# Kernel tuning notes

Measured on AMD Instinct MI355X. Metric: run time of the kernel, lower is better.

## Reference

```python
import jax, jax.numpy as jnp
import numpy as np

N_LAYERS = 10


def _rel_graph_conv(x, src, dst, etype, W_rel, W_loop, b):
    # x: [N, h]; W_rel: [R, h, h] (per-relation weight), DGL low_mem style:
    # project all nodes by all relations, then gather per edge by (etype, src).
    xr = jnp.einsum('ni,rio->rno', x, W_rel)          # [R, N, h]
    m = xr[etype, src]                                 # [E, h] per-edge messages
    agg = jax.ops.segment_sum(m, dst, num_segments=x.shape[0])  # sum aggregation
    # DGL RelGraphConv defaults: self_loop=True, bias=True, no activation
    return agg + x @ W_loop + b


def setup_inputs() -> dict:
    key = jax.random.key(0)
    ks = jax.random.split(key, 12)
    N, E, F, H, R = 100000, 600000, 64, 128, 8
    inp = {
        'feats': jax.random.normal(ks[0], (N, F), dtype=jnp.float32),
        'src': jax.random.randint(ks[1], (E,), 0, N, dtype=jnp.int32),
        'dst': jax.random.randint(ks[2], (E,), 0, N, dtype=jnp.int32),
        'etype': jax.random.randint(ks[3], (E,), 0, R, dtype=jnp.int32),
    }
    s = 0.05
    inp['W_in'] = jax.random.normal(ks[4], (F, H), dtype=jnp.float32) * s
    inp['b_in'] = jnp.zeros((H,), dtype=jnp.float32)
    # stacked params for 10 layer-dependent GCNConv layers
    inp['W_rel'] = jax.random.normal(ks[5], (N_LAYERS, R, H, H), dtype=jnp.float32) * s
    inp['W_loop'] = jax.random.normal(ks[6], (N_LAYERS, H, H), dtype=jnp.float32) * s
    inp['b_rel'] = jnp.zeros((N_LAYERS, H), dtype=jnp.float32)
    inp['W_u1'] = jax.random.normal(ks[7], (N_LAYERS, 2 * H, 2 * H), dtype=jnp.float32) * s  # Linear(h+h, 2h)
    inp['b_u1'] = jnp.zeros((N_LAYERS, 2 * H), dtype=jnp.float32)
    inp['W_u2'] = jax.random.normal(ks[8], (N_LAYERS, 3 * H, H), dtype=jnp.float32) * s      # Linear(h+2h, h)
    inp['b_u2'] = jnp.zeros((N_LAYERS, H), dtype=jnp.float32)
    return inp


def reference(feats, src, dst, etype, W_in, b_in, W_rel, W_loop, b_rel, W_u1, b_u1, W_u2, b_u2):
    act = jnp.tanh  # activation_dict['tanh']
    x = act(feats @ W_in + b_in)  # conv_input
    for l in range(N_LAYERS):
        msg = _rel_graph_conv(x, src, dst, etype, W_rel[l], W_loop[l], b_rel[l])
        mid = act(jnp.concatenate([x, msg], axis=1) @ W_u1[l] + b_u1[l])
        out = jnp.concatenate([x, mid], axis=1) @ W_u2[l] + b_u2[l]
        x = act(out)
    return x
```

## Files before the change

### kernel.cpp

```cpp
#include <hip/hip_runtime.h>
#include <cstddef>


#define HID 128
#define NREL 8
#define NL 10

typedef __attribute__((ext_vector_type(8))) __bf16 bf16x8;
typedef __attribute__((ext_vector_type(4))) float f32x4;

__device__ __forceinline__ float fast_tanh(float x) {
  float cx = fminf(fmaxf(x, -10.f), 10.f);
  float z = exp2f(cx * 2.8853900817779268f);
  return (z - 1.f) * __builtin_amdgcn_rcpf(z + 1.f);
}

__global__ __launch_bounds__(256) void k_transpose(const float* __restrict__ W,
                                                   __bf16* __restrict__ Wt,
                                                   int K, int Nc,
                                                   int inDiv, int inScale, int inOff,
                                                   int outDiv, int outScale, int outOff) {
  __shared__ float t[32][33];
  int z = blockIdx.z;
  int zi = (z / inDiv) * inScale + (z % inDiv) + inOff;
  int zo = (z / outDiv) * outScale + (z % outDiv) + outOff;
  const float* Wz = W + (size_t)zi * K * Nc;
  __bf16* Wtz = Wt + (size_t)zo * K * Nc;
  int n0 = blockIdx.x * 32, k0 = blockIdx.y * 32;
#pragma unroll
  for (int i = 0; i < 4; i++) {
    int k = k0 + threadIdx.y + i * 8;
    int n = n0 + threadIdx.x;
    t[threadIdx.y + i * 8][threadIdx.x] = Wz[(size_t)k * Nc + n];
  }
  __syncthreads();
#pragma unroll
  for (int i = 0; i < 4; i++) {
    int n = n0 + threadIdx.y + i * 8;
    int k = k0 + threadIdx.x;
    Wtz[(size_t)n * K + k] = (__bf16)t[threadIdx.x][threadIdx.y + i * 8];
  }
}

__global__ __launch_bounds__(256) void k_fold_wu1(const float* __restrict__ Wu1,
                                                  const float* __restrict__ Wloop,
                                                  __bf16* __restrict__ wt) {
  int l = blockIdx.y;
  int n0 = blockIdx.x * 32;
  const float* wu1 = Wu1 + (size_t)l * 256 * 256;
  const float* wl = Wloop + (size_t)l * 128 * 128;
  __bf16* wtl = wt + (size_t)l * 256 * 256;
  __shared__ float bot[128][33];
  for (int t = threadIdx.x; t < 128 * 32; t += 256) {
    int j = t >> 5, c = t & 31;
    bot[j][c] = wu1[(size_t)(128 + j) * 256 + n0 + c];
  }
  __syncthreads();
  int k = threadIdx.x & 127;
  int half = threadIdx.x >> 7;
  float acc[16];
#pragma unroll
  for (int c = 0; c < 16; c++) acc[c] = 0.f;
  for (int j = 0; j < 128; j++) {
    float w = wl[(size_t)k * 128 + j];
#pragma unroll
    for (int c = 0; c < 16; c++) acc[c] += w * bot[j][half * 16 + c];
  }
#pragma unroll
  for (int c = 0; c < 16; c++) {
    int n = n0 + half * 16 + c;
    wtl[(size_t)n * 256 + k] = (__bf16)(wu1[(size_t)k * 256 + n] + acc[c]);
  }
}

__global__ __launch_bounds__(256) void k_cvt(const float* __restrict__ x,
                                             __bf16* __restrict__ y, int n4) {
  int i = blockIdx.x * 256 + threadIdx.x;
  if (i < n4) {
    float4 f = ((const float4*)x)[i];
    __bf16 o[4] = {(__bf16)f.x, (__bf16)f.y, (__bf16)f.z, (__bf16)f.w};
    *(uint2*)(y + (size_t)i * 4) = *(uint2*)o;
  }
}

__global__ __launch_bounds__(256) void k_zero(int* __restrict__ p, int n) {
  for (int i = blockIdx.x * 256 + threadIdx.x; i < n; i += gridDim.x * 256) p[i] = 0;
}

__global__ __launch_bounds__(256) void k_hist_row(const int* __restrict__ dst,
                                                  int E, int* __restrict__ rowCnt) {
  int e = blockIdx.x * 256 + threadIdx.x;
  if (e < E) atomicAdd(&rowCnt[dst[e]], 1);
}

__global__ __launch_bounds__(256) void k_flag(const int* __restrict__ et,
                                              const int* __restrict__ src,
                                              int E, int N,
                                              int* __restrict__ F0,
                                              int* __restrict__ F1) {
  int e = blockIdx.x * 256 + threadIdx.x;
  if (e < E) {
    int r = et[e];
    (r < 4 ? F0 : F1)[(r & 3) * N + src[e]] = 1;
  }
}

__global__ __launch_bounds__(256) void k_srcof(const int* __restrict__ F,
                                               const int* __restrict__ P,
                                               int n, int N, int* __restrict__ srcOf) {
  int i = blockIdx.x * 256 + threadIdx.x;
  if (i < n && F[i]) srcOf[P[i]] = i % N;
}

__global__ __launch_bounds__(256) void k_scan_part(const int* __restrict__ cntArr,
                                                   int nb, int* __restrict__ thrPre,
                                                   int* __restrict__ blkSum) {
  __shared__ int sdata[256];
  int tid = threadIdx.x;
  int gtid = blockIdx.x * 256 + tid;
  int tot = gridDim.x * 256;
  int chunk = (nb + tot - 1) / tot;
  int lo = gtid * chunk, hi = min(nb, lo + chunk);
  int s = 0;
  for (int i = lo; i < hi; i++) s += cntArr[i];
  sdata[tid] = s;
  __syncthreads();
#pragma unroll
  for (int off = 1; off < 256; off <<= 1) {
    int t = (tid >= off) ? sdata[tid - off] : 0;
    __syncthreads();
    sdata[tid] += t;
    __syncthreads();
  }
  thrPre[gtid] = sdata[tid] - s;
  if (tid == 255) blkSum[blockIdx.x] = sdata[255];
}

__global__ __launch_bounds__(256) void k_scan_mid(const int* __restrict__ blkSum,
                                                  int nblk, int nb,
                                                  int* __restrict__ blkOff,
                                                  int* __restrict__ pre) {
  __shared__ int part[256];
  int tid = threadIdx.x;
  part[tid] = (tid < nblk) ? blkSum[tid] : 0;
  __syncthreads();
  if (tid == 0) {
    int a = 0;
    for (int i = 0; i < nblk; i++) { int v = part[i]; part[i] = a; a += v; }
    pre[nb] = a;
  }
  __syncthreads();
  if (tid < nblk) blkOff[tid] = part[tid];
}

__global__ __launch_bounds__(256) void k_scan_fin(const int* __restrict__ cntArr,
                                                  int nb,
                                                  const int* __restrict__ thrPre,
                                                  const int* __restrict__ blkOff,
                                                  int* __restrict__ pre,
                                                  int* __restrict__ cur) {
  int tid = threadIdx.x;
  int gtid = blockIdx.x * 256 + tid;
  int tot = gridDim.x * 256;
  int chunk = (nb + tot - 1) / tot;
  int lo = gtid * chunk, hi = min(nb, lo + chunk);
  int run = blkOff[blockIdx.x] + thrPre[gtid];
  for (int i = lo; i < hi; i++) {
    pre[i] = run;
    if (cur) cur[i] = run;
    run += cntArr[i];
  }
}

__global__ __launch_bounds__(256) void k_place_row(const int* __restrict__ et,
                                                   const int* __restrict__ src,
                                                   const int* __restrict__ dst,
                                                   const int* __restrict__ P0,
                                                   const int* __restrict__ P1,
                                                   int* __restrict__ rowCur,
                                                   int* __restrict__ epk, int E, int N) {
  int e = blockIdx.x * 256 + threadIdx.x;
  if (e < E) {
    int p = atomicAdd(&rowCur[dst[e]], 1);
    int r = et[e];
    int half = r >> 2;
    const int* P = half ? P1 : P0;
    int zrow = P[(r & 3) * N + src[e]];
    epk[p] = zrow | (half << 19);
  }
}

__global__ __launch_bounds__(256) void seg_sum(
    const __bf16* __restrict__ Zc, const int* __restrict__ rowStart,
    const int* __restrict__ epk, const float* __restrict__ b_rel_l,
    __bf16* __restrict__ msgb, int N, int half) {
  int t16 = threadIdx.x & 15;
  int d = blockIdx.x * 16 + (threadIdx.x >> 4);
  if (d >= N) return;

  float acc[8];
  if (b_rel_l) {
#pragma unroll
    for (int z = 0; z < 8; z++) acc[z] = b_rel_l[t16 * 8 + z];
  } else {
    bf16x8 mv = *(const bf16x8*)(msgb + (size_t)d * HID + t16 * 8);
#pragma unroll
    for (int z = 0; z < 8; z++) acc[z] = (float)mv[z];
  }

  const int lo = rowStart[d], hi = rowStart[d + 1];
  for (int e0 = lo; e0 < hi; e0 += 4) {
    bf16x8 v[4];
    int take[4];
#pragma unroll
    for (int u = 0; u < 4; u++) {
      int e = e0 + u;
      int in = e < hi;
      int p = epk[in ? e : lo];
      int zrow = p & 0x7FFFF;
      v[u] = *(const bf16x8*)(Zc + (size_t)zrow * HID + t16 * 8);
      take[u] = in && ((p >> 19) == half);
    }
#pragma unroll
    for (int u = 0; u < 4; u++) {
      if (take[u]) {
#pragma unroll
        for (int z = 0; z < 8; z++) acc[z] += (float)v[u][z];
      }
    }
  }

  bf16x8 o;
#pragma unroll
  for (int z = 0; z < 8; z++) o[z] = (__bf16)acc[z];
  *(bf16x8*)(msgb + (size_t)d * HID + t16 * 8) = o;
}

__global__ __launch_bounds__(512, 2) void gemm_gather(
    const __bf16* __restrict__ X, const __bf16* __restrict__ Wt4,
    const int* __restrict__ srcOf, const int* __restrict__ Pf,
    __bf16* __restrict__ Zc, int N) {
  constexpr int K = 128, NS = 4;
  __shared__ __bf16 As[2][256][32];
  __shared__ __bf16 Bs[2][128][32];

  const int tid = threadIdx.x;
  int colt, mrow;
  {
    const int gx = gridDim.x;
    const int nb = gx * gridDim.y;
    const int id = blockIdx.x + blockIdx.y * gx;
    const int q = nb >> 3, r8 = nb & 7;
    const int xcd = id & 7, i = id >> 3;
    const int wk = (xcd < r8) ? (xcd * (q + 1) + i)
                              : (r8 * (q + 1) + (xcd - r8) * q + i);
    colt = wk % gx;
    mrow = wk / gx;
  }
  const int rel = colt;
  const int base = Pf[rel * N];
  const int nxt = Pf[(rel + 1) * N];
  const int cnt = nxt - base;
  const int m0 = mrow * 256;
  if (m0 >= cnt) return;
  const __bf16* Bt = Wt4 + (size_t)rel * K * 128;

  const int w = tid >> 6, lane = tid & 63;
  const int cA0 = w * 128 + lane;
  const int rA0 = cA0 >> 2, sA0 = cA0 & 3;
  const int cA1 = cA0 + 64;
  const int rA1 = cA1 >> 2, sA1 = cA1 & 3;
  const int cB = w * 64 + lane;
  const int rB = cB >> 2, sB = cB & 3;

  const int src0 = srcOf[min(base + m0 + rA0, nxt - 1)];
  const int src1 = srcOf[min(base + m0 + rA1, nxt - 1)];
  const __bf16* a0 = X + (size_t)src0 * K + sA0 * 8;
  const __bf16* a1 = X + (size_t)src1 * K + sA1 * 8;

  auto stage_step = [&](int b, int ks) {
    const __bf16* g = Bt + (size_t)rB * K + ks * 32 + sB * 8;
    __builtin_amdgcn_global_load_lds(
        (const __attribute__((address_space(1))) void*)g,
        (__attribute__((address_space(3))) void*)(&Bs[b][0][0] + (size_t)w * 512),
        16, 0, 0);
    __builtin_amdgcn_global_load_lds(
        (const __attribute__((address_space(1))) void*)(a0 + ks * 32),
        (__attribute__((address_space(3))) void*)(&As[b][0][0] + (size_t)(w * 2 + 0) * 512),
        16, 0, 0);
    __builtin_amdgcn_global_load_lds(
        (const __attribute__((address_space(1))) void*)(a1 + ks * 32),
        (__attribute__((address_space(3))) void*)(&As[b][0][0] + (size_t)(w * 2 + 1) * 512),
        16, 0, 0);
  };

  const int ml = lane & 15, q2 = lane >> 4;
  const int wr = (w >> 1) * 64, wc = (w & 1) * 64;

  f32x4 acc[4][4];
#pragma unroll
  for (int i = 0; i < 4; i++)
#pragma unroll
    for (int j = 0; j < 4; j++)
#pragma unroll
      for (int r = 0; r < 4; r++) acc[i][j][r] = 0.f;

  stage_step(0, 0);
  stage_step(1, 1);

#pragma unroll
  for (int ks = 0; ks < NS; ks++) {
    const int cur = ks & 1;
    if (ks + 1 < NS) asm volatile("s_waitcnt vmcnt(3)" ::: "memory");
    else             asm volatile("s_waitcnt vmcnt(0)" ::: "memory");
    asm volatile("s_barrier" ::: "memory");

    bf16x8 af[4], bfr[4];
#pragma unroll
    for (int i = 0; i < 4; i++)
      af[i] = *(const bf16x8*)(&As[cur][wr + i * 16 + ml][q2 * 8]);
#pragma unroll
    for (int j = 0; j < 4; j++)
      bfr[j] = *(const bf16x8*)(&Bs[cur][wc + j * 16 + ml][q2 * 8]);
#pragma unroll
    for (int i = 0; i < 4; i++)
#pragma unroll
      for (int j = 0; j < 4; j++)
        acc[i][j] = __builtin_amdgcn_mfma_f32_16x16x32_bf16(af[i], bfr[j],
                                                            acc[i][j], 0, 0, 0);

    asm volatile("s_barrier" ::: "memory");
    if (ks + 2 < NS) stage_step(cur, ks + 2);
  }

#pragma unroll
  for (int i = 0; i < 4; i++) {
#pragma unroll
    for (int r = 0; r < 4; r++) {
      int lrow = m0 + wr + i * 16 + q2 * 4 + r;
      if (lrow >= cnt) continue;
#pragma unroll
      for (int j = 0; j < 4; j++) {
        int col = wc + j * 16 + ml;
        Zc[(size_t)(base + lrow) * HID + col] = (__bf16)acc[i][j][r];
      }
    }
  }
}

template <int K, int K0, int MINW>
__global__ __launch_bounds__(512, MINW) void gemm_lds(
    const __bf16* __restrict__ A0, const __bf16* __restrict__ A1,
    const __bf16* __restrict__ Bt, const float* __restrict__ bias,
    __bf16* __restrict__ Cb, float* __restrict__ Cf,
    int M, int Nc, int act) {
  constexpr int NS = K / 32;
  constexpr int NS0 = K0 / 32;
  constexpr int K1 = (K - K0) > 0 ? (K - K0) : 1;
  __shared__ __bf16 As[2][256][32];
  __shared__ __bf16 Bs[2][128][32];

  const int tid = threadIdx.x;
  int colt, mrow;
  {
    const int gx = gridDim.x;
    const int nb = gx * gridDim.y;
    const int id = blockIdx.x + blockIdx.y * gx;
    const int q = nb >> 3, r8 = nb & 7;
    const int xcd = id & 7, i = id >> 3;
    const int wk = (xcd < r8) ? (xcd * (q + 1) + i)
                              : (r8 * (q + 1) + (xcd - r8) * q + i);
    colt = wk % gx;
    mrow = wk / gx;
  }
  const int m0 = mrow * 256;
  const int bn0 = colt * 128;

  const int w = tid >> 6;
  const int lane = tid & 63;

  const int cA0 = w * 128 + lane;
  const int rA0 = cA0 >> 2, sA0 = cA0 & 3;
  const int cA1 = cA0 + 64;
  const int rA1 = cA1 >> 2, sA1 = cA1 & 3;
  const int cB = w * 64 + lane;
  const int rB = cB >> 2, sB = cB & 3;

  auto stage_step = [&](int b, int ks) {
    {
      const __bf16* g = Bt + (size_t)(bn0 + rB) * K + ks * 32 + sB * 8;
      __builtin_amdgcn_global_load_lds(
          (const __attribute__((address_space(1))) void*)g,
          (__attribute__((address_space(3))) void*)(&Bs[b][0][0] + (size_t)w * 512),
          16, 0, 0);
    }
    if (ks < NS0) {
      const __bf16* g0 = A0 + (size_t)(m0 + rA0) * K0 + ks * 32 + sA0 * 8;
      __builtin_amdgcn_global_load_lds(
          (const __attribute__((address_space(1))) void*)g0,
          (__attribute__((address_space(3))) void*)(&As[b][0][0] + (size_t)(w * 2 + 0) * 512),
          16, 0, 0);
      const __bf16* g1 = A0 + (size_t)(m0 + rA1) * K0 + ks * 32 + sA1 * 8;
      __builtin_amdgcn_global_load_lds(
          (const __attribute__((address_space(1))) void*)g1,
          (__attribute__((address_space(3))) void*)(&As[b][0][0] + (size_t)(w * 2 + 1) * 512),
          16, 0, 0);
    } else {
      const __bf16* g0 = A1 + (size_t)(m0 + rA0) * K1 + (ks - NS0) * 32 + sA0 * 8;
      __builtin_amdgcn_global_load_lds(
          (const __attribute__((address_space(1))) void*)g0,
          (__attribute__((address_space(3))) void*)(&As[b][0][0] + (size_t)(w * 2 + 0) * 512),
          16, 0, 0);
      const __bf16* g1 = A1 + (size_t)(m0 + rA1) * K1 + (ks - NS0) * 32 + sA1 * 8;
      __builtin_amdgcn_global_load_lds(
          (const __attribute__((address_space(1))) void*)g1,
          (__attribute__((address_space(3))) void*)(&As[b][0][0] + (size_t)(w * 2 + 1) * 512),
          16, 0, 0);
    }
  };

  const int ml = lane & 15, q2 = lane >> 4;
  const int wr = (w >> 1) * 64;
  const int wc = (w & 1) * 64;

  f32x4 acc[4][4];
#pragma unroll
  for (int i = 0; i < 4; i++)
#pragma unroll
    for (int j = 0; j < 4; j++)
#pragma unroll
      for (int r = 0; r < 4; r++) acc[i][j][r] = 0.f;

  stage_step(0, 0);
  if (NS > 1) stage_step(1, 1);

#pragma unroll
  for (int ks = 0; ks < NS; ks++) {
    const int cur = ks & 1;
    if (ks + 1 < NS) asm volatile("s_waitcnt vmcnt(3)" ::: "memory");
    else             asm volatile("s_waitcnt vmcnt(0)" ::: "memory");
    asm volatile("s_barrier" ::: "memory");

    bf16x8 af[4], bfr[4];
#pragma unroll
    for (int i = 0; i < 4; i++)
      af[i] = *(const bf16x8*)(&As[cur][wr + i * 16 + ml][q2 * 8]);
#pragma unroll
    for (int j = 0; j < 4; j++)
      bfr[j] = *(const bf16x8*)(&Bs[cur][wc + j * 16 + ml][q2 * 8]);
#pragma unroll
    for (int i = 0; i < 4; i++)
#pragma unroll
      for (int j = 0; j < 4; j++)
        acc[i][j] = __builtin_amdgcn_mfma_f32_16x16x32_bf16(af[i], bfr[j],
                                                            acc[i][j], 0, 0, 0);

    asm volatile("s_barrier" ::: "memory");
    if (ks + 2 < NS) stage_step(cur, ks + 2);
  }

#pragma unroll
  for (int i = 0; i < 4; i++) {
#pragma unroll
    for (int r = 0; r < 4; r++) {
      int grow = m0 + wr + i * 16 + q2 * 4 + r;
      if (grow >= M) continue;
#pragma unroll
      for (int j = 0; j < 4; j++) {
        int col = bn0 + wc + j * 16 + ml;
        float v = acc[i][j][r];
        if (bias) v += bias[col];
        if (act) v = fast_tanh(v);
        if (Cb) Cb[(size_t)grow * Nc + col] = (__bf16)v;
        if (Cf) Cf[(size_t)grow * Nc + col] = v;
      }
    }
  }
}

extern "C" void kernel_launch(void* const* d_in, const int* in_sizes, int n_in,
                              void* d_out, int out_size, void* d_ws, size_t ws_size,
                              hipStream_t stream) {
  const float* feats  = (const float*)d_in[0];
  const int*   src    = (const int*)d_in[1];
  const int*   dst    = (const int*)d_in[2];
  const int*   etype  = (const int*)d_in[3];
  const float* W_in   = (const float*)d_in[4];
  const float* b_in   = (const float*)d_in[5];
  const float* W_rel  = (const float*)d_in[6];
  const float* W_loop = (const float*)d_in[7];
  const float* b_rel  = (const float*)d_in[8];
  const float* W_u1   = (const float*)d_in[9];
  const float* b_u1   = (const float*)d_in[10];
  const float* W_u2   = (const float*)d_in[11];
  const float* b_u2   = (const float*)d_in[12];

  const int E = in_sizes[1];
  const int N = in_sizes[0] / 64;
  const int TS = HID * HID;

  __bf16* xb0  = (__bf16*)d_ws;
  __bf16* xb1  = xb0 + (size_t)N * HID;
  __bf16* msgb = xb1 + (size_t)N * HID;
  __bf16* U    = msgb + (size_t)N * HID;
  __bf16* Z    = U;
  __bf16* mid  = U;
  __bf16* featsb = U;
  __bf16* wt_in = U + (size_t)N * 640;
  __bf16* wt_z0 = wt_in + 128 * 64;
  __bf16* wt_z1 = wt_z0 + (size_t)10 * 4 * TS;
  __bf16* wt_u1 = wt_z1 + (size_t)10 * 4 * TS;
  __bf16* wt_u2 = wt_u1 + (size_t)10 * 256 * 256;
  int* rowCnt   = (int*)(wt_u2 + (size_t)10 * 128 * 384);
  int* rowStart = rowCnt + N;
  int* rowCur   = rowStart + N + 1;
  int* epk      = rowCur + N;
  int* thrPre   = epk + E;
  int* blkSum   = thrPre + 256 * 256;
  int* blkOff   = blkSum + 256;
  int* F0       = blkOff + 256;
  int* F1       = F0 + 4 * N;
  int* P0       = F1 + 4 * N;
  int* P1       = P0 + 4 * N + 1;
  int* S0       = P1 + 4 * N + 1;
  int* S1       = S0 + 4 * N;

  k_transpose<<<dim3(4, 2, 1), dim3(32, 8), 0, stream>>>(W_in, wt_in, 64, 128,
                                                         1, 1, 0, 1, 1, 0);
  k_transpose<<<dim3(4, 4, 40), dim3(32, 8), 0, stream>>>(W_rel, wt_z0, 128, 128,
                                                          4, 8, 0, 4, 4, 0);
  k_transpose<<<dim3(4, 4, 40), dim3(32, 8), 0, stream>>>(W_rel, wt_z1, 128, 128,
                                                          4, 8, 4, 4, 4, 0);
  k_transpose<<<dim3(8, 8, 10), dim3(32, 8), 0, stream>>>(W_u1, wt_u1, 256, 256,
                                                          1, 1, 0, 1, 1, 0);
  k_fold_wu1<<<dim3(8, 10), dim3(256), 0, stream>>>(W_u1, W_loop, wt_u1);
  k_transpose<<<dim3(4, 12, 10), dim3(32, 8), 0, stream>>>(W_u2, wt_u2, 384, 128,
                                                           1, 1, 0, 1, 1, 0);
  k_cvt<<<(N * 64 / 4 + 255) / 256, 256, 0, stream>>>(feats, featsb, N * 64 / 4);

  k_zero<<<128, 256, 0, stream>>>(rowCnt, N);
  k_zero<<<256, 256, 0, stream>>>(F0, 4 * N);
  k_zero<<<256, 256, 0, stream>>>(F1, 4 * N);
  k_hist_row<<<(E + 255) / 256, 256, 0, stream>>>(dst, E, rowCnt);
  k_flag<<<(E + 255) / 256, 256, 0, stream>>>(etype, src, E, N, F0, F1);
  k_scan_part<<<256, 256, 0, stream>>>(rowCnt, N, thrPre, blkSum);
  k_scan_mid<<<1, 256, 0, stream>>>(blkSum, 256, N, blkOff, rowStart);
  k_scan_fin<<<256, 256, 0, stream>>>(rowCnt, N, thrPre, blkOff, rowStart, rowCur);
  k_scan_part<<<256, 256, 0, stream>>>(F0, 4 * N, thrPre, blkSum);
  k_scan_mid<<<1, 256, 0, stream>>>(blkSum, 256, 4 * N, blkOff, P0);
  k_scan_fin<<<256, 256, 0, stream>>>(F0, 4 * N, thrPre, blkOff, P0, nullptr);
  k_scan_part<<<256, 256, 0, stream>>>(F1, 4 * N, thrPre, blkSum);
  k_scan_mid<<<1, 256, 0, stream>>>(blkSum, 256, 4 * N, blkOff, P1);
  k_scan_fin<<<256, 256, 0, stream>>>(F1, 4 * N, thrPre, blkOff, P1, nullptr);
  k_srcof<<<(4 * N + 255) / 256, 256, 0, stream>>>(F0, P0, 4 * N, N, S0);
  k_srcof<<<(4 * N + 255) / 256, 256, 0, stream>>>(F1, P1, 4 * N, N, S1);
  k_place_row<<<(E + 255) / 256, 256, 0, stream>>>(etype, src, dst, P0, P1,
                                                   rowCur, epk, E, N);

  const dim3 blk(512);
  const int gm = (N + 255) / 256;
  const dim3 gseg((N + 15) / 16);

  gemm_lds<64, 64, 2><<<dim3(1, gm), blk, 0, stream>>>(
      featsb, featsb, wt_in, b_in, xb0, nullptr, N, HID, 1);

  for (int l = 0; l < NL; l++) {
    const __bf16* xin = (l & 1) ? xb1 : xb0;
    __bf16* xout = (l & 1) ? xb0 : xb1;

    gemm_gather<<<dim3(4, gm), blk, 0, stream>>>(
        xin, wt_z0 + (size_t)l * 4 * TS, S0, P0, Z, N);
    seg_sum<<<gseg, dim3(256), 0, stream>>>(Z, rowStart, epk,
                                            b_rel + (size_t)l * HID,
                                            msgb, N, 0);
    gemm_gather<<<dim3(4, gm), blk, 0, stream>>>(
        xin, wt_z1 + (size_t)l * 4 * TS, S1, P1, Z, N);
    seg_sum<<<gseg, dim3(256), 0, stream>>>(Z, rowStart, epk, nullptr,
                                            msgb, N, 1);

    gemm_lds<256, 128, 2><<<dim3(2, gm), blk, 0, stream>>>(
        xin, msgb, wt_u1 + (size_t)l * 256 * 256, b_u1 + (size_t)l * 256,
        mid, nullptr, N, 256, 1);

    gemm_lds<384, 128, 2><<<dim3(1, gm), blk, 0, stream>>>(
        xin, mid, wt_u2 + (size_t)l * HID * 384, b_u2 + (size_t)l * HID,
        (l == NL - 1) ? nullptr : xout,
        (l == NL - 1) ? (float*)d_out : nullptr,
        N, HID, 1);
  }
}
```

Measured before the change: 2.294 ms.

## Merge two relation halves into one gather-GEMM and add a 128-row GEMM variant

Per layer, the two four-relation gather-GEMM and segment-sum passes become a single pass over all eight relations. Z holds every relation's projected rows at once, so segment-sum reads each edge list once and drops the half-flag filtering and the read-modify-write of msgb. A new 256-thread, 128-row-tile GEMM kernel is added and used for the input projection and the 384-K output GEMM to give more blocks on narrow-N GEMMs. The trade-off is a larger Z scratch buffer (up to 8N rows, which must still fit the 19-bit row index) and different occupancy characteristics.

```diff
diff --git a/kernel.cpp b/kernel.cpp
--- a/kernel.cpp
+++ b/kernel.cpp
@@ -95,14 +95,9 @@
 
 __global__ __launch_bounds__(256) void k_flag(const int* __restrict__ et,
                                               const int* __restrict__ src,
-                                              int E, int N,
-                                              int* __restrict__ F0,
-                                              int* __restrict__ F1) {
+                                              int E, int N, int* __restrict__ F) {
   int e = blockIdx.x * 256 + threadIdx.x;
-  if (e < E) {
-    int r = et[e];
-    (r < 4 ? F0 : F1)[(r & 3) * N + src[e]] = 1;
-  }
+  if (e < E) F[(size_t)et[e] * N + src[e]] = 1;
 }
 
 __global__ __launch_bounds__(256) void k_srcof(const int* __restrict__ F,
@@ -175,38 +170,27 @@
 __global__ __launch_bounds__(256) void k_place_row(const int* __restrict__ et,
                                                    const int* __restrict__ src,
                                                    const int* __restrict__ dst,
-                                                   const int* __restrict__ P0,
-                                                   const int* __restrict__ P1,
+                                                   const int* __restrict__ P,
                                                    int* __restrict__ rowCur,
                                                    int* __restrict__ epk, int E, int N) {
   int e = blockIdx.x * 256 + threadIdx.x;
   if (e < E) {
     int p = atomicAdd(&rowCur[dst[e]], 1);
-    int r = et[e];
-    int half = r >> 2;
-    const int* P = half ? P1 : P0;
-    int zrow = P[(r & 3) * N + src[e]];
-    epk[p] = zrow | (half << 19);
+    epk[p] = P[(size_t)et[e] * N + src[e]];
   }
 }
 
 __global__ __launch_bounds__(256) void seg_sum(
     const __bf16* __restrict__ Zc, const int* __restrict__ rowStart,
     const int* __restrict__ epk, const float* __restrict__ b_rel_l,
-    __bf16* __restrict__ msgb, int N, int half) {
+    __bf16* __restrict__ msgb, int N) {
   int t16 = threadIdx.x & 15;
   int d = blockIdx.x * 16 + (threadIdx.x >> 4);
   if (d >= N) return;
 
   float acc[8];
-  if (b_rel_l) {
-#pragma unroll
-    for (int z = 0; z < 8; z++) acc[z] = b_rel_l[t16 * 8 + z];
-  } else {
-    bf16x8 mv = *(const bf16x8*)(msgb + (size_t)d * HID + t16 * 8);
-#pragma unroll
-    for (int z = 0; z < 8; z++) acc[z] = (float)mv[z];
-  }
+#pragma unroll
+  for (int z = 0; z < 8; z++) acc[z] = b_rel_l[t16 * 8 + z];
 
   const int lo = rowStart[d], hi = rowStart[d + 1];
   for (int e0 = lo; e0 < hi; e0 += 4) {
@@ -216,10 +200,9 @@
     for (int u = 0; u < 4; u++) {
       int e = e0 + u;
       int in = e < hi;
-      int p = epk[in ? e : lo];
-      int zrow = p & 0x7FFFF;
+      int zrow = epk[in ? e : lo];
       v[u] = *(const bf16x8*)(Zc + (size_t)zrow * HID + t16 * 8);
-      take[u] = in && ((p >> 19) == half);
+      take[u] = in;
     }
 #pragma unroll
     for (int u = 0; u < 4; u++) {
@@ -237,7 +220,7 @@
 }
 
 __global__ __launch_bounds__(512, 2) void gemm_gather(
-    const __bf16* __restrict__ X, const __bf16* __restrict__ Wt4,
+    const __bf16* __restrict__ X, const __bf16* __restrict__ Wt8,
     const int* __restrict__ srcOf, const int* __restrict__ Pf,
     __bf16* __restrict__ Zc, int N) {
   constexpr int K = 128, NS = 4;
@@ -258,12 +241,12 @@
     mrow = wk / gx;
   }
   const int rel = colt;
-  const int base = Pf[rel * N];
-  const int nxt = Pf[(rel + 1) * N];
+  const int base = Pf[(size_t)rel * N];
+  const int nxt = Pf[(size_t)(rel + 1) * N];
   const int cnt = nxt - base;
   const int m0 = mrow * 256;
   if (m0 >= cnt) return;
-  const __bf16* Bt = Wt4 + (size_t)rel * K * 128;
+  const __bf16* Bt = Wt8 + (size_t)rel * K * 128;
 
   const int w = tid >> 6, lane = tid & 63;
   const int cA0 = w * 128 + lane;
@@ -438,6 +421,137 @@
   for (int ks = 0; ks < NS; ks++) {
     const int cur = ks & 1;
     if (ks + 1 < NS) asm volatile("s_waitcnt vmcnt(3)" ::: "memory");
+    else             asm volatile("s_waitcnt vmcnt(0)" ::: "memory");
+    asm volatile("s_barrier" ::: "memory");
+
+    bf16x8 af[4], bfr[4];
+#pragma unroll
+    for (int i = 0; i < 4; i++)
+      af[i] = *(const bf16x8*)(&As[cur][wr + i * 16 + ml][q2 * 8]);
+#pragma unroll
+    for (int j = 0; j < 4; j++)
+      bfr[j] = *(const bf16x8*)(&Bs[cur][wc + j * 16 + ml][q2 * 8]);
+#pragma unroll
+    for (int i = 0; i < 4; i++)
+#pragma unroll
+      for (int j = 0; j < 4; j++)
+        acc[i][j] = __builtin_amdgcn_mfma_f32_16x16x32_bf16(af[i], bfr[j],
+                                                            acc[i][j], 0, 0, 0);
+
+    asm volatile("s_barrier" ::: "memory");
+    if (ks + 2 < NS) stage_step(cur, ks + 2);
+  }
+
+#pragma unroll
+  for (int i = 0; i < 4; i++) {
+#pragma unroll
+    for (int r = 0; r < 4; r++) {
+      int grow = m0 + wr + i * 16 + q2 * 4 + r;
+      if (grow >= M) continue;
+#pragma unroll
+      for (int j = 0; j < 4; j++) {
+        int col = bn0 + wc + j * 16 + ml;
+        float v = acc[i][j][r];
+        if (bias) v += bias[col];
+        if (act) v = fast_tanh(v);
+        if (Cb) Cb[(size_t)grow * Nc + col] = (__bf16)v;
+        if (Cf) Cf[(size_t)grow * Nc + col] = v;
+      }
+    }
+  }
+}
+
+template <int K, int K0, int MINW>
+__global__ __launch_bounds__(256, MINW) void gemm_lds128(
+    const __bf16* __restrict__ A0, const __bf16* __restrict__ A1,
+    const __bf16* __restrict__ Bt, const float* __restrict__ bias,
+    __bf16* __restrict__ Cb, float* __restrict__ Cf,
+    int M, int Nc, int act) {
+  constexpr int NS = K / 32;
+  constexpr int NS0 = K0 / 32;
+  constexpr int K1 = (K - K0) > 0 ? (K - K0) : 1;
+  __shared__ __bf16 As[2][128][32];
+  __shared__ __bf16 Bs[2][128][32];
+
+  const int tid = threadIdx.x;
+  int colt, mrow;
+  {
+    const int gx = gridDim.x;
+    const int nb = gx * gridDim.y;
+    const int id = blockIdx.x + blockIdx.y * gx;
+    const int q = nb >> 3, r8 = nb & 7;
+    const int xcd = id & 7, i = id >> 3;
+    const int wk = (xcd < r8) ? (xcd * (q + 1) + i)
+                              : (r8 * (q + 1) + (xcd - r8) * q + i);
+    colt = wk % gx;
+    mrow = wk / gx;
+  }
+  const int m0 = mrow * 128;
+  const int bn0 = colt * 128;
+
+  const int w = tid >> 6;
+  const int lane = tid & 63;
+
+  const int c0 = w * 128 + lane;
+  const int r0 = c0 >> 2, s0 = c0 & 3;
+  const int c1 = c0 + 64;
+  const int r1 = c1 >> 2, s1 = c1 & 3;
+
+  auto stage_step = [&](int b, int ks) {
+    const __bf16* gB0 = Bt + (size_t)(bn0 + r0) * K + ks * 32 + s0 * 8;
+    __builtin_amdgcn_global_load_lds(
+        (const __attribute__((address_space(1))) void*)gB0,
+        (__attribute__((address_space(3))) void*)(&Bs[b][0][0] + (size_t)(w * 2 + 0) * 512),
+        16, 0, 0);
+    const __bf16* gB1 = Bt + (size_t)(bn0 + r1) * K + ks * 32 + s1 * 8;
+    __builtin_amdgcn_global_load_lds(
+        (const __attribute__((address_space(1))) void*)gB1,
+        (__attribute__((address_space(3))) void*)(&Bs[b][0][0] + (size_t)(w * 2 + 1) * 512),
+        16, 0, 0);
+    if (ks < NS0) {
+      const __bf16* g0 = A0 + (size_t)(m0 + r0) * K0 + ks * 32 + s0 * 8;
+      __builtin_amdgcn_global_load_lds(
+          (const __attribute__((address_space(1))) void*)g0,
+          (__attribute__((address_space(3))) void*)(&As[b][0][0] + (size_t)(w * 2 + 0) * 512),
+          16, 0, 0);
+      const __bf16* g1 = A0 + (size_t)(m0 + r1) * K0 + ks * 32 + s1 * 8;
+      __builtin_amdgcn_global_load_lds(
+          (const __attribute__((address_space(1))) void*)g1,
+          (__attribute__((address_space(3))) void*)(&As[b][0][0] + (size_t)(w * 2 + 1) * 512),
+          16, 0, 0);
+    } else {
+      const __bf16* g0 = A1 + (size_t)(m0 + r0) * K1 + (ks - NS0) * 32 + s0 * 8;
+      __builtin_amdgcn_global_load_lds(
+          (const __attribute__((address_space(1))) void*)g0,
+          (__attribute__((address_space(3))) void*)(&As[b][0][0] + (size_t)(w * 2 + 0) * 512),
+          16, 0, 0);
+      const __bf16* g1 = A1 + (size_t)(m0 + r1) * K1 + (ks - NS0) * 32 + s1 * 8;
+      __builtin_amdgcn_global_load_lds(
+          (const __attribute__((address_space(1))) void*)g1,
+          (__attribute__((address_space(3))) void*)(&As[b][0][0] + (size_t)(w * 2 + 1) * 512),
+          16, 0, 0);
+    }
+  };
+
+  const int ml = lane & 15, q2 = lane >> 4;
+  const int wr = (w >> 1) * 64;
+  const int wc = (w & 1) * 64;
+
+  f32x4 acc[4][4];
+#pragma unroll
+  for (int i = 0; i < 4; i++)
+#pragma unroll
+    for (int j = 0; j < 4; j++)
+#pragma unroll
+      for (int r = 0; r < 4; r++) acc[i][j][r] = 0.f;
+
+  stage_step(0, 0);
+  if (NS > 1) stage_step(1, 1);
+
+#pragma unroll
+  for (int ks = 0; ks < NS; ks++) {
+    const int cur = ks & 1;
+    if (ks + 1 < NS) asm volatile("s_waitcnt vmcnt(4)" ::: "memory");
     else             asm volatile("s_waitcnt vmcnt(0)" ::: "memory");
     asm volatile("s_barrier" ::: "memory");
 
@@ -507,9 +621,8 @@
   __bf16* mid  = U;
   __bf16* featsb = U;
   __bf16* wt_in = U + (size_t)N * 640;
-  __bf16* wt_z0 = wt_in + 128 * 64;
-  __bf16* wt_z1 = wt_z0 + (size_t)10 * 4 * TS;
-  __bf16* wt_u1 = wt_z1 + (size_t)10 * 4 * TS;
+  __bf16* wt_z  = wt_in + 128 * 64;
+  __bf16* wt_u1 = wt_z + (size_t)10 * 8 * TS;
   __bf16* wt_u2 = wt_u1 + (size_t)10 * 256 * 256;
   int* rowCnt   = (int*)(wt_u2 + (size_t)10 * 128 * 384);
   int* rowStart = rowCnt + N;
@@ -518,19 +631,14 @@
   int* thrPre   = epk + E;
   int* blkSum   = thrPre + 256 * 256;
   int* blkOff   = blkSum + 256;
-  int* F0       = blkOff + 256;
-  int* F1       = F0 + 4 * N;
-  int* P0       = F1 + 4 * N;
-  int* P1       = P0 + 4 * N + 1;
-  int* S0       = P1 + 4 * N + 1;
-  int* S1       = S0 + 4 * N;
+  int* F        = blkOff + 256;
+  int* P        = F + 8 * N;
+  int* S        = P + 8 * N + 1;
 
   k_transpose<<<dim3(4, 2, 1), dim3(32, 8), 0, stream>>>(W_in, wt_in, 64, 128,
                                                          1, 1, 0, 1, 1, 0);
-  k_transpose<<<dim3(4, 4, 40), dim3(32, 8), 0, stream>>>(W_rel, wt_z0, 128, 128,
-                                                          4, 8, 0, 4, 4, 0);
-  k_transpose<<<dim3(4, 4, 40), dim3(32, 8), 0, stream>>>(W_rel, wt_z1, 128, 128,
-                                                          4, 8, 4, 4, 4, 0);
+  k_transpose<<<dim3(4, 4, 80), dim3(32, 8), 0, stream>>>(W_rel, wt_z, 128, 128,
+                                                          1, 1, 0, 1, 1, 0);
   k_transpose<<<dim3(8, 8, 10), dim3(32, 8), 0, stream>>>(W_u1, wt_u1, 256, 256,
                                                           1, 1, 0, 1, 1, 0);
   k_fold_wu1<<<dim3(8, 10), dim3(256), 0, stream>>>(W_u1, W_loop, wt_u1);
@@ -539,50 +647,40 @@
   k_cvt<<<(N * 64 / 4 + 255) / 256, 256, 0, stream>>>(feats, featsb, N * 64 / 4);
 
   k_zero<<<128, 256, 0, stream>>>(rowCnt, N);
-  k_zero<<<256, 256, 0, stream>>>(F0, 4 * N);
-  k_zero<<<256, 256, 0, stream>>>(F1, 4 * N);
+  k_zero<<<512, 256, 0, stream>>>(F, 8 * N);
   k_hist_row<<<(E + 255) / 256, 256, 0, stream>>>(dst, E, rowCnt);
-  k_flag<<<(E + 255) / 256, 256, 0, stream>>>(etype, src, E, N, F0, F1);
+  k_flag<<<(E + 255) / 256, 256, 0, stream>>>(etype, src, E, N, F);
   k_scan_part<<<256, 256, 0, stream>>>(rowCnt, N, thrPre, blkSum);
   k_scan_mid<<<1, 256, 0, stream>>>(blkSum, 256, N, blkOff, rowStart);
   k_scan_fin<<<256, 256, 0, stream>>>(rowCnt, N, thrPre, blkOff, rowStart, rowCur);
-  k_scan_part<<<256, 256, 0, stream>>>(F0, 4 * N, thrPre, blkSum);
-  k_scan_mid<<<1, 256, 0, stream>>>(blkSum, 256, 4 * N, blkOff, P0);
-  k_scan_fin<<<256, 256, 0, stream>>>(F0, 4 * N, thrPre, blkOff, P0, nullptr);
-  k_scan_part<<<256, 256, 0, stream>>>(F1, 4 * N, thrPre, blkSum);
-  k_scan_mid<<<1, 256, 0, stream>>>(blkSum, 256, 4 * N, blkOff, P1);
-  k_scan_fin<<<256, 256, 0, stream>>>(F1, 4 * N, thrPre, blkOff, P1, nullptr);
-  k_srcof<<<(4 * N + 255) / 256, 256, 0, stream>>>(F0, P0, 4 * N, N, S0);
-  k_srcof<<<(4 * N + 255) / 256, 256, 0, stream>>>(F1, P1, 4 * N, N, S1);
-  k_place_row<<<(E + 255) / 256, 256, 0, stream>>>(etype, src, dst, P0, P1,
+  k_scan_part<<<256, 256, 0, stream>>>(F, 8 * N, thrPre, blkSum);
+  k_scan_mid<<<1, 256, 0, stream>>>(blkSum, 256, 8 * N, blkOff, P);
+  k_scan_fin<<<256, 256, 0, stream>>>(F, 8 * N, thrPre, blkOff, P, nullptr);
+  k_srcof<<<(8 * N + 255) / 256, 256, 0, stream>>>(F, P, 8 * N, N, S);
+  k_place_row<<<(E + 255) / 256, 256, 0, stream>>>(etype, src, dst, P,
                                                    rowCur, epk, E, N);
 
-  const dim3 blk(512);
   const int gm = (N + 255) / 256;
+  const int gm128 = (N + 127) / 128;
   const dim3 gseg((N + 15) / 16);
 
-  gemm_lds<64, 64, 2><<<dim3(1, gm), blk, 0, stream>>>(
+  gemm_lds128<64, 64, 2><<<dim3(1, gm128), dim3(256), 0, stream>>>(
       featsb, featsb, wt_in, b_in, xb0, nullptr, N, HID, 1);
 
   for (int l = 0; l < NL; l++) {
     const __bf16* xin = (l & 1) ? xb1 : xb0;
     __bf16* xout = (l & 1) ? xb0 : xb1;
 
-    gemm_gather<<<dim3(4, gm), blk, 0, stream>>>(
-        xin, wt_z0 + (size_t)l * 4 * TS, S0, P0, Z, N);
+    gemm_gather<<<dim3(8, gm), dim3(512), 0, stream>>>(
+        xin, wt_z + (size_t)l * 8 * TS, S, P, Z, N);
     seg_sum<<<gseg, dim3(256), 0, stream>>>(Z, rowStart, epk,
-                                            b_rel + (size_t)l * HID,
-                                            msgb, N, 0);
-    gemm_gather<<<dim3(4, gm), blk, 0, stream>>>(
-        xin, wt_z1 + (size_t)l * 4 * TS, S1, P1, Z, N);
-    seg_sum<<<gseg, dim3(256), 0, stream>>>(Z, rowStart, epk, nullptr,
-                                            msgb, N, 1);
-
-    gemm_lds<256, 128, 2><<<dim3(2, gm), blk, 0, stream>>>(
+                                            b_rel + (size_t)l * HID, msgb, N);
+
+    gemm_lds<256, 128, 2><<<dim3(2, gm), dim3(512), 0, stream>>>(
         xin, msgb, wt_u1 + (size_t)l * 256 * 256, b_u1 + (size_t)l * 256,
         mid, nullptr, N, 256, 1);
 
-    gemm_lds<384, 128, 2><<<dim3(1, gm), blk, 0, stream>>>(
+    gemm_lds128<384, 128, 2><<<dim3(1, gm128), dim3(256), 0, stream>>>(
         xin, mid, wt_u2 + (size_t)l * HID * 384, b_u2 + (size_t)l * HID,
         (l == NL - 1) ? nullptr : xout,
         (l == NL - 1) ? (float*)d_out : nullptr,
```

Result: faster. 1.920 ms (-16.3%).
